# Performance work log

Measured on AMD Instinct MI355X. Metric: run time of the kernel, lower is better.

The kernel has to match this reference:

```python
import jax, jax.numpy as jnp
import numpy as np

BATCH, LENGTH, INPUT, HIDDEN = 64, 2048, 128, 256

def setup_inputs() -> dict:
    key = jax.random.key(0)
    k1, k2, k3, k4 = jax.random.split(key, 4)
    x = jax.random.normal(k1, (BATCH, LENGTH, INPUT), dtype=jnp.float32)
    h = jnp.zeros((BATCH, HIDDEN), dtype=jnp.float32)
    W_x = jax.random.normal(k2, (HIDDEN, INPUT), dtype=jnp.float32)
    W_h = jax.random.normal(k3, (HIDDEN, HIDDEN), dtype=jnp.float32)
    b_h = jax.random.normal(k4, (HIDDEN,), dtype=jnp.float32)
    return {"x": x, "h": h, "W_x": W_x, "W_h": W_h, "b_h": b_h}

def reference(x, h, W_x, W_h, b_h):
    # x: [b, l, i]; h: [b, hidden]; returns [l, b, hidden] (matches torch forward)
    # Pre-compute input projection for all timesteps in one GEMM: [b, l, hidden]
    xw = jnp.einsum('bli,hi->blh', x, W_x)
    xw_t = jnp.swapaxes(xw, 0, 1)  # [l, b, hidden]

    def step(h, xw_step):
        h_new = jnp.tanh(xw_step + h @ W_h.T + b_h)
        return h_new, h_new

    _, output = jax.lax.scan(step, h, xw_t)
    return output  # [l, b, hidden]
```

## Files before the change

kernel.cpp:

```cpp
#include <hip/hip_runtime.h>

#define BATCH 64
#define LEN   2048
#define NIN   128
#define NH    256

typedef float f32x4 __attribute__((ext_vector_type(4)));
typedef float f32x2 __attribute__((ext_vector_type(2)));

__device__ __forceinline__ float tanh_xla_fma_f32(float x) {
  const float kClamp = 7.99881172180175781f;
  float xc = fmaxf(x, -kClamp);
  xc = fminf(xc, kClamp);
  float x2 = xc * xc;
  float num = fmaf(x2, -2.76076847742355e-16f, 2.00018790482477e-13f);
  num = fmaf(x2, num, -8.60467152213735e-11f);
  num = fmaf(x2, num, 5.12229709037114e-08f);
  num = fmaf(x2, num, 1.48572235717979e-05f);
  num = fmaf(x2, num, 6.37261928875436e-04f);
  num = fmaf(x2, num, 4.89352455891786e-03f);
  num = xc * num;
  float den = fmaf(x2, 1.19825839466702e-06f, 1.18534705686654e-04f);
  den = fmaf(x2, den, 2.26843463243900e-03f);
  den = fmaf(x2, den, 4.89352518554385e-03f);
  float r = num / den;
  return (fabsf(x) < 0.0004f) ? x : r;
}

#define PINV(v) asm("" : "+v"(v));

#define RLANE(val, q) \
  __uint_as_float(__builtin_amdgcn_readlane(__float_as_uint(val), (q)))

#define REPQ48(M) M(0) M(1) M(2) M(3) M(4) M(5) M(6) M(7) \
  M(8) M(9) M(10) M(11) M(12) M(13) M(14) M(15) \
  M(16) M(17) M(18) M(19) M(20) M(21) M(22) M(23) \
  M(24) M(25) M(26) M(27) M(28) M(29) M(30) M(31) \
  M(32) M(33) M(34) M(35) M(36) M(37) M(38) M(39) \
  M(40) M(41) M(42) M(43) M(44) M(45) M(46) M(47)
#define REPQ16(M) M(48) M(49) M(50) M(51) M(52) M(53) M(54) M(55) \
  M(56) M(57) M(58) M(59) M(60) M(61) M(62) M(63)
#define REPX32(M) M(0) M(1) M(2) M(3) M(4) M(5) M(6) M(7) \
  M(8) M(9) M(10) M(11) M(12) M(13) M(14) M(15) \
  M(16) M(17) M(18) M(19) M(20) M(21) M(22) M(23) \
  M(24) M(25) M(26) M(27) M(28) M(29) M(30) M(31)

#define WQ_DECL(n) f32x4 wq##n;
#define WQ_LOAD(n) wq##n = wrow[n]; PINV(wq##n)
#define AQ_DECL(n) float aq##n##x, aq##n##y, aq##n##z, aq##n##w;
#define AQ_LOAD(n) { f32x4 v = wrow[n]; \
  asm("v_accvgpr_write_b32 %0, %1" : "=a"(aq##n##x) : "v"(v.x)); \
  asm("v_accvgpr_write_b32 %0, %1" : "=a"(aq##n##y) : "v"(v.y)); \
  asm("v_accvgpr_write_b32 %0, %1" : "=a"(aq##n##z) : "v"(v.z)); \
  asm("v_accvgpr_write_b32 %0, %1" : "=a"(aq##n##w) : "v"(v.w)); }

#define STEPV(n) \
  acc = fmaf(RLANE(hq.x, n), wq##n.x, acc); \
  acc = fmaf(RLANE(hq.y, n), wq##n.y, acc); \
  acc = fmaf(RLANE(hq.z, n), wq##n.z, acc); \
  acc = fmaf(RLANE(hq.w, n), wq##n.w, acc);
#define STEPA(n) { float t0, t1, t2, t3; \
  asm volatile("v_accvgpr_read_b32 %0, %1" : "=v"(t0) : "a"(aq##n##x)); \
  asm volatile("v_accvgpr_read_b32 %0, %1" : "=v"(t1) : "a"(aq##n##y)); \
  asm volatile("v_accvgpr_read_b32 %0, %1" : "=v"(t2) : "a"(aq##n##z)); \
  asm volatile("v_accvgpr_read_b32 %0, %1" : "=v"(t3) : "a"(aq##n##w)); \
  acc = fmaf(RLANE(hq.x, n), t0, acc); \
  acc = fmaf(RLANE(hq.y, n), t1, acc); \
  acc = fmaf(RLANE(hq.z, n), t2, acc); \
  acc = fmaf(RLANE(hq.w, n), t3, acc); }

#define XSTEP(n) \
  acc = fmaf(RLANE(xv.x, 2*(n)    ), wq##n.x, acc); \
  acc = fmaf(RLANE(xv.y, 2*(n)    ), wq##n.y, acc); \
  acc = fmaf(RLANE(xv.x, 2*(n) + 1), wq##n.z, acc); \
  acc = fmaf(RLANE(xv.y, 2*(n) + 1), wq##n.w, acc);

constexpr int LC = 128;

__global__ __launch_bounds__(256, 2)
void xw_kernel(const float* __restrict__ x, const float* __restrict__ Wx,
               float* __restrict__ out) {
  const int j    = threadIdx.x;
  const int lane = j & 63;
  const int b    = blockIdx.x & (BATCH - 1);
  const int lt   = blockIdx.x >> 6;

  const f32x4* wrow = (const f32x4*)&Wx[(size_t)j * NIN];
  REPX32(WQ_DECL)
  REPX32(WQ_LOAD)

  const float* xr = x + ((size_t)b * LEN + (size_t)lt * LC) * NIN;
  float* op = out + ((size_t)lt * LC * BATCH + b) * NH + j;

  f32x2 xv = *(const f32x2*)(xr + 2 * lane);
  for (int ll = 0; ll < LC; ++ll) {
    const int ln = (ll + 1 < LC) ? (ll + 1) : ll;
    f32x2 xnext = *(const f32x2*)(xr + (size_t)ln * NIN + 2 * lane);
    float acc = 0.0f;
    REPX32(XSTEP)
    op[(size_t)ll * BATCH * NH] = acc;
    xv = xnext;
  }
}

__global__ __launch_bounds__(256, 1)
void rnn_kernel(const float* __restrict__ Wh, const float* __restrict__ bh,
                const float* __restrict__ h0, float* __restrict__ io) {
  const int b    = blockIdx.x;
  const int j    = threadIdx.x;
  const int lane = j & 63;

  __shared__ __align__(16) float hbuf[2][NH];

  const f32x4* wrow = (const f32x4*)&Wh[(size_t)j * NH];
  REPQ48(WQ_DECL)
  REPQ16(AQ_DECL)
  REPQ48(WQ_LOAD)
  REPQ16(AQ_LOAD)

  const float bias = bh[j];
  hbuf[0][j] = h0[b * NH + j];
  __syncthreads();

  float* p = io + (size_t)b * NH + j;
  const size_t stride = (size_t)BATCH * NH;

  float xw = p[0];
  int cur = 0;

  for (int l = 0; l < LEN; ++l) {
    const int ln = (l + 1 < LEN) ? (l + 1) : l;
    const float xw_next = p[(size_t)ln * stride];

    const f32x4 hq = *(const f32x4*)&hbuf[cur][4 * lane];
    float acc = 0.0f;
    REPQ48(STEPV)
    REPQ16(STEPA)

    float pre;
    {
#pragma clang fp contract(off)
      pre = (xw + acc) + bias;
    }
    const float hn = tanh_xla_fma_f32(pre);

    p[(size_t)l * stride] = hn;
    hbuf[cur ^ 1][j] = hn;

    asm volatile("s_waitcnt lgkmcnt(0)" ::: "memory");
    __builtin_amdgcn_s_barrier();
    asm volatile("" ::: "memory");

    cur ^= 1;
    xw = xw_next;
  }
}

extern "C" void kernel_launch(void* const* d_in, const int* in_sizes, int n_in,
                              void* d_out, int out_size, void* d_ws, size_t ws_size,
                              hipStream_t stream) {
  const float* x  = (const float*)d_in[0];
  const float* h0 = (const float*)d_in[1];
  const float* Wx = (const float*)d_in[2];
  const float* Wh = (const float*)d_in[3];
  const float* bh = (const float*)d_in[4];
  for (int i = 0; i < n_in; ++i) {
    switch (in_sizes[i]) {
      case 16777216: x  = (const float*)d_in[i]; break;
      case 16384:    h0 = (const float*)d_in[i]; break;
      case 32768:    Wx = (const float*)d_in[i]; break;
      case 65536:    Wh = (const float*)d_in[i]; break;
      case 256:      bh = (const float*)d_in[i]; break;
      default: break;
    }
  }
  float* out = (float*)d_out;

  xw_kernel<<<dim3((LEN / LC) * BATCH), dim3(256), 0, stream>>>(x, Wx, out);
  rnn_kernel<<<dim3(BATCH), dim3(256), 0, stream>>>(Wh, bh, h0, out);
}
```

Before: 2.617 ms.

## Split recurrent matvec across two thread halves with a shared-memory partial sum

The recurrent kernel now launches 512 threads per batch row. Each half holds half of the W_h row in VGPRs, so the AGPR-spilled weight path and its accvgpr reads go away. The first half computes its partial dot product and writes it to shared memory. After an added barrier, the second half adds its own half and applies tanh. Because the two halves run one after the other around that extra barrier, the per-step critical path gains a sync and may not get shorter.

After: 4.336 ms. 1.66x slower.

```diff
diff --git a/kernel.cpp b/kernel.cpp
--- a/kernel.cpp
+++ b/kernel.cpp
@@ -32,14 +32,6 @@
 #define RLANE(val, q) \
   __uint_as_float(__builtin_amdgcn_readlane(__float_as_uint(val), (q)))
 
-#define REPQ48(M) M(0) M(1) M(2) M(3) M(4) M(5) M(6) M(7) \
-  M(8) M(9) M(10) M(11) M(12) M(13) M(14) M(15) \
-  M(16) M(17) M(18) M(19) M(20) M(21) M(22) M(23) \
-  M(24) M(25) M(26) M(27) M(28) M(29) M(30) M(31) \
-  M(32) M(33) M(34) M(35) M(36) M(37) M(38) M(39) \
-  M(40) M(41) M(42) M(43) M(44) M(45) M(46) M(47)
-#define REPQ16(M) M(48) M(49) M(50) M(51) M(52) M(53) M(54) M(55) \
-  M(56) M(57) M(58) M(59) M(60) M(61) M(62) M(63)
 #define REPX32(M) M(0) M(1) M(2) M(3) M(4) M(5) M(6) M(7) \
   M(8) M(9) M(10) M(11) M(12) M(13) M(14) M(15) \
   M(16) M(17) M(18) M(19) M(20) M(21) M(22) M(23) \
@@ -47,27 +39,12 @@
 
 #define WQ_DECL(n) f32x4 wq##n;
 #define WQ_LOAD(n) wq##n = wrow[n]; PINV(wq##n)
-#define AQ_DECL(n) float aq##n##x, aq##n##y, aq##n##z, aq##n##w;
-#define AQ_LOAD(n) { f32x4 v = wrow[n]; \
-  asm("v_accvgpr_write_b32 %0, %1" : "=a"(aq##n##x) : "v"(v.x)); \
-  asm("v_accvgpr_write_b32 %0, %1" : "=a"(aq##n##y) : "v"(v.y)); \
-  asm("v_accvgpr_write_b32 %0, %1" : "=a"(aq##n##z) : "v"(v.z)); \
-  asm("v_accvgpr_write_b32 %0, %1" : "=a"(aq##n##w) : "v"(v.w)); }
 
-#define STEPV(n) \
+#define HSTEP(n) \
   acc = fmaf(RLANE(hq.x, n), wq##n.x, acc); \
   acc = fmaf(RLANE(hq.y, n), wq##n.y, acc); \
   acc = fmaf(RLANE(hq.z, n), wq##n.z, acc); \
   acc = fmaf(RLANE(hq.w, n), wq##n.w, acc);
-#define STEPA(n) { float t0, t1, t2, t3; \
-  asm volatile("v_accvgpr_read_b32 %0, %1" : "=v"(t0) : "a"(aq##n##x)); \
-  asm volatile("v_accvgpr_read_b32 %0, %1" : "=v"(t1) : "a"(aq##n##y)); \
-  asm volatile("v_accvgpr_read_b32 %0, %1" : "=v"(t2) : "a"(aq##n##z)); \
-  asm volatile("v_accvgpr_read_b32 %0, %1" : "=v"(t3) : "a"(aq##n##w)); \
-  acc = fmaf(RLANE(hq.x, n), t0, acc); \
-  acc = fmaf(RLANE(hq.y, n), t1, acc); \
-  acc = fmaf(RLANE(hq.z, n), t2, acc); \
-  acc = fmaf(RLANE(hq.w, n), t3, acc); }
 
 #define XSTEP(n) \
   acc = fmaf(RLANE(xv.x, 2*(n)    ), wq##n.x, acc); \
@@ -103,23 +80,26 @@
   }
 }
 
-__global__ __launch_bounds__(256, 1)
+__global__ __launch_bounds__(512, 1)
 void rnn_kernel(const float* __restrict__ Wh, const float* __restrict__ bh,
                 const float* __restrict__ h0, float* __restrict__ io) {
   const int b    = blockIdx.x;
-  const int j    = threadIdx.x;
-  const int lane = j & 63;
+  const int tid  = threadIdx.x;
+  const int j    = tid & (NH - 1);
+  const int s    = tid >> 8;
+  const int lane = tid & 63;
 
   __shared__ __align__(16) float hbuf[2][NH];
+  __shared__ __align__(16) float part[NH];
 
-  const f32x4* wrow = (const f32x4*)&Wh[(size_t)j * NH];
-  REPQ48(WQ_DECL)
-  REPQ16(AQ_DECL)
-  REPQ48(WQ_LOAD)
-  REPQ16(AQ_LOAD)
+  const f32x4* wrow = (const f32x4*)&Wh[(size_t)j * NH + (s ? 128 : 0)];
+  REPX32(WQ_DECL)
+  REPX32(WQ_LOAD)
 
   const float bias = bh[j];
-  hbuf[0][j] = h0[b * NH + j];
+  const int hoff = (s ? 128 : 0) + 4 * (lane & 31);
+
+  if (tid < NH) hbuf[0][tid] = h0[b * NH + tid];
   __syncthreads();
 
   float* p = io + (size_t)b * NH + j;
@@ -129,23 +109,37 @@
   int cur = 0;
 
   for (int l = 0; l < LEN; ++l) {
+    if (s == 0) {
+      const f32x4 hq = *(const f32x4*)&hbuf[cur][hoff];
+      float acc = 0.0f;
+      REPX32(HSTEP)
+      part[j] = acc;
+    } else {
+      const int ln = (l + 1 < LEN) ? (l + 1) : l;
+      xw = (l == 0) ? xw : xw;
+    }
     const int ln = (l + 1 < LEN) ? (l + 1) : l;
     const float xw_next = p[(size_t)ln * stride];
 
-    const f32x4 hq = *(const f32x4*)&hbuf[cur][4 * lane];
-    float acc = 0.0f;
-    REPQ48(STEPV)
-    REPQ16(STEPA)
+    asm volatile("s_waitcnt lgkmcnt(0)" ::: "memory");
+    __builtin_amdgcn_s_barrier();
+    asm volatile("" ::: "memory");
 
-    float pre;
-    {
+    if (s == 1) {
+      const f32x4 hq = *(const f32x4*)&hbuf[cur][hoff];
+      float acc = part[j];
+      REPX32(HSTEP)
+
+      float pre;
+      {
 #pragma clang fp contract(off)
-      pre = (xw + acc) + bias;
+        pre = (xw + acc) + bias;
+      }
+      const float hn = tanh_xla_fma_f32(pre);
+
+      p[(size_t)l * stride] = hn;
+      hbuf[cur ^ 1][j] = hn;
     }
-    const float hn = tanh_xla_fma_f32(pre);
-
-    p[(size_t)l * stride] = hn;
-    hbuf[cur ^ 1][j] = hn;
 
     asm volatile("s_waitcnt lgkmcnt(0)" ::: "memory");
     __builtin_amdgcn_s_barrier();
@@ -177,5 +171,5 @@
   float* out = (float*)d_out;
 
   xw_kernel<<<dim3((LEN / LC) * BATCH), dim3(256), 0, stream>>>(x, Wx, out);
-  rnn_kernel<<<dim3(BATCH), dim3(256), 0, stream>>>(Wh, bh, h0, out);
+  rnn_kernel<<<dim3(BATCH), dim3(512), 0, stream>>>(Wh, bh, h0, out);
 }
```
